# Optimization experiments

Measured on AMD Instinct MI355X. Metric: run time of the kernel, lower is better.

The kernel has to match this reference:

```python
import jax, jax.numpy as jnp
import numpy as np

B, S, D, H = 1, 4096, 1024, 16
HD = D // H

def setup_inputs() -> dict:
    key = jax.random.key(0)
    ks = jax.random.split(key, 6)
    scale = 0.02
    return {
        "x":  jax.random.normal(ks[0], (B, S, D), dtype=jnp.float32),
        "Wq": jax.random.normal(ks[1], (D, D), dtype=jnp.float32) * scale,
        "Wk": jax.random.normal(ks[2], (D, D), dtype=jnp.float32) * scale,
        "Wv": jax.random.normal(ks[3], (D, D), dtype=jnp.float32) * scale,
        "Wo": jax.random.normal(ks[4], (D, D), dtype=jnp.float32) * scale,
        "bo": jnp.zeros((D,), dtype=jnp.float32),
    }

def reference(x, Wq, Wk, Wv, Wo, bo):
    b, s, d = x.shape
    # torch Linear: y = x @ W.T (weights stored [out,in])
    def proj(W):
        return (x @ W.T).reshape(b, s, H, HD).transpose(0, 2, 1, 3)  # [b,h,s,hd]
    q, k, v = proj(Wq), proj(Wk), proj(Wv)
    scores = jnp.einsum('bhqd,bhkd->bhqk', q, k)  # [b,h,s,s]
    causal = jnp.tril(jnp.ones((s, s), dtype=bool))
    scores = jnp.where(causal, scores, -jnp.inf)
    weights = jax.nn.softmax(scores / np.sqrt(HD).astype(np.float32), axis=-1)
    ctx = jnp.einsum('bhqk,bhkd->bhqd', weights, v)
    ctx = ctx.transpose(0, 2, 1, 3).reshape(b, s, d)
    return ctx @ Wo.T + bo
```

## Files before the change

kernel.cpp:

```cpp
#include <hip/hip_runtime.h>
#include <stdint.h>

typedef unsigned short u16;
typedef __attribute__((ext_vector_type(4))) unsigned short u16x4;
typedef __attribute__((ext_vector_type(8))) unsigned short u16x8;
typedef __attribute__((ext_vector_type(8))) __bf16 bf16x8;
typedef __attribute__((ext_vector_type(4))) float f32x4;
typedef __attribute__((ext_vector_type(16))) float f32x16;

#define S_LEN 4096
#define D_DIM 1024
#define NH    16
#define HD    64

__device__ __forceinline__ u16 f2bf(float f) {
  return __builtin_bit_cast(u16, (__bf16)f);
}
__device__ __forceinline__ float bf2f(u16 v) {
  return __builtin_bit_cast(float, (uint32_t)v << 16);
}
__device__ __forceinline__ bf16x8 bc(u16x8 v) { return __builtin_bit_cast(bf16x8, v); }
__device__ __forceinline__ float fexp2(float x) { return __builtin_amdgcn_exp2f(x); }

__device__ __forceinline__ void gload16(const u16* g, u16* l) {
  __builtin_amdgcn_global_load_lds((__attribute__((address_space(1))) void*)g,
                                   (__attribute__((address_space(3))) void*)l, 16, 0, 0);
}

__global__ __launch_bounds__(256) void conv_all_kernel(const float* __restrict__ x,
                                                       const float* __restrict__ Wq,
                                                       const float* __restrict__ Wk,
                                                       const float* __restrict__ Wv,
                                                       const float* __restrict__ Wo,
                                                       u16* __restrict__ Xb, u16* __restrict__ Wqb,
                                                       u16* __restrict__ Wkb, u16* __restrict__ Wvb,
                                                       u16* __restrict__ Wob) {
  int blk = blockIdx.x;
  const float* src;
  u16* dst;
  int i;
  if (blk < 4096) { src = x; dst = Xb; i = blk * 256 + threadIdx.x; }
  else {
    int wi = (blk - 4096) >> 10;
    int lb = (blk - 4096) & 1023;
    src = (wi == 0) ? Wq : (wi == 1) ? Wk : (wi == 2) ? Wv : Wo;
    dst = (wi == 0) ? Wqb : (wi == 1) ? Wkb : (wi == 2) ? Wvb : Wob;
    i = lb * 256 + threadIdx.x;
  }
  f32x4 v = ((const f32x4*)src)[i];
  u16x4 o;
  o[0] = f2bf(v[0]); o[1] = f2bf(v[1]); o[2] = f2bf(v[2]); o[3] = f2bf(v[3]);
  ((u16x4*)dst)[i] = o;
}

__device__ __forceinline__ void gemm_core(const u16* __restrict__ A,
                                          const u16* __restrict__ W,
                                          int m0, int n0, int Kd,
                                          u16* As, u16* Bs, f32x4 acc[4][4]) {
  const int tid  = threadIdx.x;
  const int lane = tid & 63;
  const int wv   = tid >> 6;
  const int wr   = wv >> 1, wc = wv & 1;
  const int b    = lane & 15, quad = lane >> 4;
  const int lrow = lane >> 2;
  const int cg   = ((lane & 3) - (lrow >> 1)) & 3;
  const int goff = ((quad + (b >> 1)) & 3) * 8;

  const u16* ga0 = A + (size_t)(m0 + wv * 16 + lrow) * Kd + cg * 8;
  const u16* ga1 = A + (size_t)(m0 + 64 + wv * 16 + lrow) * Kd + cg * 8;
  const u16* gb0 = W + (size_t)(n0 + wv * 16 + lrow) * Kd + cg * 8;
  const u16* gb1 = W + (size_t)(n0 + 64 + wv * 16 + lrow) * Kd + cg * 8;
  u16* la0 = As + wv * 512;
  u16* la1 = As + 2048 + wv * 512;
  u16* lb0 = Bs + wv * 512;
  u16* lb1 = Bs + 2048 + wv * 512;

  auto stage = [&](int k0, int bsel) {
    gload16(ga0 + k0, la0 + bsel * 4096);
    gload16(ga1 + k0, la1 + bsel * 4096);
    gload16(gb0 + k0, lb0 + bsel * 4096);
    gload16(gb1 + k0, lb1 + bsel * 4096);
  };

  stage(0, 0);
  int buf = 0;
  for (int k0 = 0; k0 < Kd; k0 += 32) {
    __syncthreads();
    if (k0 + 32 < Kd) stage(k0 + 32, buf ^ 1);

    const u16* AB = As + buf * 4096;
    const u16* BB = Bs + buf * 4096;
    u16x8 af[4], bw[4];
#pragma unroll
    for (int i = 0; i < 4; ++i) {
      af[i] = *(const u16x8*)(AB + (wr * 64 + i * 16 + b) * 32 + goff);
      bw[i] = *(const u16x8*)(BB + (wc * 64 + i * 16 + b) * 32 + goff);
    }
#pragma unroll
    for (int i = 0; i < 4; ++i)
#pragma unroll
      for (int j = 0; j < 4; ++j)
        acc[i][j] = __builtin_amdgcn_mfma_f32_16x16x32_bf16(bc(af[i]), bc(bw[j]), acc[i][j], 0, 0, 0);
    buf ^= 1;
  }
}

__global__ __launch_bounds__(256) void gemm_qkv_kernel(const u16* __restrict__ X,
                                                       const u16* __restrict__ Wq,
                                                       const u16* __restrict__ Wk,
                                                       const u16* __restrict__ Wv,
                                                       u16* __restrict__ Q,
                                                       u16* __restrict__ K,
                                                       u16* __restrict__ Vt) {
  __shared__ __align__(16) u16 As[2 * 4096];
  __shared__ __align__(16) u16 Bs[2 * 4096];
  const int z = blockIdx.z;
  const u16* W = (z == 0) ? Wq : (z == 1) ? Wk : Wv;
  const int n0 = blockIdx.x * 128, m0 = blockIdx.y * 128;

  const f32x4 zero4 = {0.f, 0.f, 0.f, 0.f};
  f32x4 acc[4][4];
#pragma unroll
  for (int i = 0; i < 4; ++i)
#pragma unroll
    for (int j = 0; j < 4; ++j) acc[i][j] = zero4;

  gemm_core(X, W, m0, n0, D_DIM, As, Bs, acc);

  const int lane = threadIdx.x & 63;
  const int wv = threadIdx.x >> 6, wr = wv >> 1, wc = wv & 1;
  const int b = lane & 15, quad = lane >> 4;

  if (z < 2) {
    u16* out = (z == 0) ? Q : K;
    const float sc = (z == 0) ? 0.18033688011112042f : 1.0f;
#pragma unroll
    for (int i = 0; i < 4; ++i)
#pragma unroll
      for (int j = 0; j < 4; ++j)
#pragma unroll
        for (int r = 0; r < 4; ++r) {
          int row = m0 + wr * 64 + i * 16 + quad * 4 + r;
          int col = n0 + wc * 64 + j * 16 + b;
          out[(size_t)row * D_DIM + col] = f2bf(acc[i][j][r] * sc);
        }
  } else {
#pragma unroll
    for (int i = 0; i < 4; ++i)
#pragma unroll
      for (int j = 0; j < 4; ++j) {
        int col = n0 + wc * 64 + j * 16 + b;
        int row = m0 + wr * 64 + i * 16 + quad * 4;
        u16x4 vv;
#pragma unroll
        for (int r = 0; r < 4; ++r) vv[r] = f2bf(acc[i][j][r]);
        *(u16x4*)(Vt + (size_t)col * S_LEN + row) = vv;
      }
  }
}

__global__ __launch_bounds__(256) void attn_kernel(const u16* __restrict__ Q,
                                                   const u16* __restrict__ K,
                                                   const u16* __restrict__ Vt,
                                                   u16* __restrict__ Opart,
                                                   float* __restrict__ ml) {
  const int u = (int)gridDim.x - 1 - (int)blockIdx.x;
  const int h = u / 80;
  const int uu = u - h * 80;
  int qt, c;
  if (uu < 8)       { qt = uu;                    c = 0; }
  else if (uu < 24) { qt = 8 + ((uu - 8) >> 1);   c = (uu - 8) & 1; }
  else if (uu < 48) { qt = 16 + (uu - 24) / 3;    c = (uu - 24) % 3; }
  else              { qt = 24 + ((uu - 48) >> 2); c = (uu - 48) & 3; }
  const int t0 = c * 16;
  const int t_end = min(t0 + 16, 2 * qt + 2);
  const int q0 = qt * 128;

  const int tid = threadIdx.x, lane = tid & 63, w = tid >> 6;
  const int half = lane >> 5;
  const int l31 = lane & 31;

  __shared__ __align__(16) u16 Ks[2][4096];
  __shared__ __align__(16) u16 Vts[2][4096];
  __shared__ __align__(16) u16 Ps[4][32 * 72];

  const int sr    = lane >> 3;
  const int srow  = w * 16 + sr;
  const int clog  = ((lane & 7) - sr) & 7;
  const u16* kgb = K + (size_t)srow * D_DIM + h * HD + clog * 8;
  const u16* vgb = Vt + (size_t)(h * HD + srow) * S_LEN + clog * 8;
  u16* const ldk = &Ks[0][0] + w * 16 * 64;
  u16* const ldv = &Vts[0][0] + w * 16 * 64;

  auto stage = [&](int t, int bsel) {
    const u16* kg = kgb + (size_t)t * 64 * D_DIM;
    const u16* vg = vgb + t * 64;
    gload16(kg, ldk + bsel * 4096);
    gload16(kg + 8 * D_DIM, ldk + bsel * 4096 + 512);
    gload16(vg, ldv + bsel * 4096);
    gload16(vg + 8 * S_LEN, ldv + bsel * 4096 + 512);
  };

  u16x8 bq[4];
  {
    const u16* qp = Q + (size_t)(q0 + w * 32 + l31) * D_DIM + h * HD + half * 8;
#pragma unroll
    for (int dt = 0; dt < 4; ++dt) bq[dt] = *(const u16x8*)(qp + dt * 16);
  }

  const f32x16 zero16 = {0.f,0.f,0.f,0.f,0.f,0.f,0.f,0.f,0.f,0.f,0.f,0.f,0.f,0.f,0.f,0.f};
  f32x16 ot[2];
  ot[0] = zero16; ot[1] = zero16;
  float m_run = -3.0e38f, l_run = 0.f;

  u16* const PsW = &Ps[w][0];
  const int qg = q0 + w * 32 + l31;
  const int qg_wmax = q0 + w * 32 + 31;

  stage(t0, 0);
  int buf = 0;

  for (int t = t0; t < t_end; ++t) {
    __syncthreads();
    if (t + 1 < t_end) stage(t + 1, buf ^ 1);

    if (t * 64 <= qg_wmax) {
      const u16* KB = &Ks[buf][0];
      const u16* VB = &Vts[buf][0];

      f32x16 s[2];
      s[0] = zero16; s[1] = zero16;
#pragma unroll
      for (int jt = 0; jt < 2; ++jt) {
        const int row = jt * 32 + l31;
#pragma unroll
        for (int dt = 0; dt < 4; ++dt) {
          u16x8 ak = *(const u16x8*)(KB + row * 64 + (((dt * 2 + half) + row) & 7) * 8);
          s[jt] = __builtin_amdgcn_mfma_f32_32x32x16_bf16(bc(ak), bc(bq[dt]), s[jt], 0, 0, 0);
        }
      }

      if (t * 64 + 63 > qg) {
#pragma unroll
        for (int jt = 0; jt < 2; ++jt) {
          const int kvb = t * 64 + jt * 32 + 4 * half;
#pragma unroll
          for (int e = 0; e < 16; ++e)
            if (kvb + (e & 3) + 8 * (e >> 2) > qg) s[jt][e] = -1.0e30f;
        }
      }

      float mx = -3.0e38f;
#pragma unroll
      for (int jt = 0; jt < 2; ++jt)
#pragma unroll
        for (int e = 0; e < 16; ++e) mx = fmaxf(mx, s[jt][e]);
      mx = fmaxf(mx, __shfl_xor(mx, 32));

      const float mn = fmaxf(m_run, mx);
      const float alpha = fexp2(m_run - mn);
      m_run = mn;

      float sum = 0.f;
#pragma unroll
      for (int jt = 0; jt < 2; ++jt)
#pragma unroll
        for (int g = 0; g < 4; ++g) {
          u16x4 pk;
#pragma unroll
          for (int r = 0; r < 4; ++r) {
            float p = fexp2(s[jt][4 * g + r] - mn);
            sum += p;
            pk[r] = f2bf(p);
          }
          *(u16x4*)(PsW + l31 * 72 + jt * 32 + 4 * half + 8 * g) = pk;
        }
      sum += __shfl_xor(sum, 32);
      l_run = l_run * alpha + sum;

      ot[0] *= alpha;
      ot[1] *= alpha;

#pragma unroll
      for (int kt = 0; kt < 4; ++kt) {
        u16x8 bp = *(const u16x8*)(PsW + l31 * 72 + kt * 16 + half * 8);
#pragma unroll
        for (int dt2 = 0; dt2 < 2; ++dt2) {
          const int row = dt2 * 32 + l31;
          u16x8 av = *(const u16x8*)(VB + row * 64 + (((kt * 2 + half) + row) & 7) * 8);
          ot[dt2] = __builtin_amdgcn_mfma_f32_32x32x16_bf16(bc(av), bc(bp), ot[dt2], 0, 0, 0);
        }
      }
    }
    buf ^= 1;
  }

  const size_t ob = (size_t)u * 8192 + (size_t)(w * 32 + l31) * 64 + 4 * half;
#pragma unroll
  for (int dt2 = 0; dt2 < 2; ++dt2)
#pragma unroll
    for (int g = 0; g < 4; ++g) {
      u16x4 ov;
#pragma unroll
      for (int r = 0; r < 4; ++r) ov[r] = f2bf(ot[dt2][4 * g + r]);
      *(u16x4*)(Opart + ob + dt2 * 32 + 8 * g) = ov;
    }
  if (lane < 32) {
    ml[(size_t)u * 256 + w * 32 + lane]       = m_run;
    ml[(size_t)u * 256 + 128 + w * 32 + lane] = l_run;
  }
}

__global__ __launch_bounds__(256) void attn_combine_kernel(const u16* __restrict__ Opart,
                                                           const float* __restrict__ ml,
                                                           u16* __restrict__ Ctx) {
  const int hq = blockIdx.x;
  const int h = hq >> 6, qt64 = hq & 63;
  const int qt = qt64 >> 1;
  int base;
  if (qt < 8)       base = qt;
  else if (qt < 16) base = 2 * qt - 8;
  else if (qt < 24) base = 3 * qt - 24;
  else              base = 4 * qt - 48;
  base += h * 80;
  const int nc = 1 + (qt >> 3);

  const int tid = threadIdx.x;
  const int row = tid >> 2;
  const int urow = (qt64 & 1) * 64 + row;
  const int dg  = (tid & 3) * 16;

  float M = -3.0e38f;
  for (int ci = 0; ci < nc; ++ci)
    M = fmaxf(M, ml[(size_t)(base + ci) * 256 + urow]);

  float L = 0.f;
  float acc[16];
#pragma unroll
  for (int i = 0; i < 16; ++i) acc[i] = 0.f;

  for (int ci = 0; ci < nc; ++ci) {
    float mp = ml[(size_t)(base + ci) * 256 + urow];
    float lp = ml[(size_t)(base + ci) * 256 + 128 + urow];
    float wgt = fexp2(mp - M);
    L += lp * wgt;
    const u16* op = Opart + (size_t)(base + ci) * 8192 + (size_t)urow * 64 + dg;
    u16x8 v0 = *(const u16x8*)op;
    u16x8 v1 = *(const u16x8*)(op + 8);
#pragma unroll
    for (int i = 0; i < 8; ++i) acc[i] += bf2f(v0[i]) * wgt;
#pragma unroll
    for (int i = 0; i < 8; ++i) acc[i + 8] += bf2f(v1[i]) * wgt;
  }
  const float inv = 1.f / L;
  u16x8 o0, o1;
#pragma unroll
  for (int i = 0; i < 8; ++i) { o0[i] = f2bf(acc[i] * inv); o1[i] = f2bf(acc[i + 8] * inv); }
  u16* dst = Ctx + (size_t)(qt64 * 64 + row) * D_DIM + h * HD + dg;
  *(u16x8*)dst = o0;
  *(u16x8*)(dst + 8) = o1;
}

__global__ __launch_bounds__(256) void gemm_out_kernel(const u16* __restrict__ Ctx,
                                                       const u16* __restrict__ Wo,
                                                       const float* __restrict__ bo,
                                                       float* __restrict__ out) {
  __shared__ __align__(16) u16 As[2 * 4096];
  __shared__ __align__(16) u16 Bs[2 * 4096];
  const int n0 = blockIdx.x * 128, m0 = blockIdx.y * 128;

  const f32x4 zero4 = {0.f, 0.f, 0.f, 0.f};
  f32x4 acc[4][4];
#pragma unroll
  for (int i = 0; i < 4; ++i)
#pragma unroll
    for (int j = 0; j < 4; ++j) acc[i][j] = zero4;

  gemm_core(Ctx, Wo, m0, n0, D_DIM, As, Bs, acc);

  const int lane = threadIdx.x & 63;
  const int wv = threadIdx.x >> 6, wr = wv >> 1, wc = wv & 1;
  const int b = lane & 15, quad = lane >> 4;

#pragma unroll
  for (int j = 0; j < 4; ++j) {
    int col = n0 + wc * 64 + j * 16 + b;
    float bias = bo[col];
#pragma unroll
    for (int i = 0; i < 4; ++i)
#pragma unroll
      for (int r = 0; r < 4; ++r) {
        int row = m0 + wr * 64 + i * 16 + quad * 4 + r;
        out[(size_t)row * D_DIM + col] = acc[i][j][r] + bias;
      }
  }
}

extern "C" void kernel_launch(void* const* d_in, const int* in_sizes, int n_in,
                              void* d_out, int out_size, void* d_ws, size_t ws_size,
                              hipStream_t stream) {
  const float* x  = (const float*)d_in[0];
  const float* Wq = (const float*)d_in[1];
  const float* Wk = (const float*)d_in[2];
  const float* Wv = (const float*)d_in[3];
  const float* Wo = (const float*)d_in[4];
  const float* bo = (const float*)d_in[5];
  float* out = (float*)d_out;

  char* ws = (char*)d_ws;
  const size_t MB = 1u << 20;
  u16*   Xb    = (u16*)(ws + 0 * MB);
  u16*   Wqb   = (u16*)(ws + 8 * MB);
  u16*   Wkb   = (u16*)(ws + 10 * MB);
  u16*   Wvb   = (u16*)(ws + 12 * MB);
  u16*   Wob   = (u16*)(ws + 14 * MB);
  u16*   Qb    = (u16*)(ws + 16 * MB);
  u16*   Kb    = (u16*)(ws + 24 * MB);
  u16*   Vtb   = (u16*)(ws + 32 * MB);
  u16*   Cxb   = (u16*)(ws + 40 * MB);
  u16*   Opart = (u16*)(ws + 48 * MB);
  float* mlbuf = (float*)(ws + 68 * MB);

  conv_all_kernel<<<8192, 256, 0, stream>>>(x, Wq, Wk, Wv, Wo, Xb, Wqb, Wkb, Wvb, Wob);

  gemm_qkv_kernel<<<dim3(D_DIM / 128, S_LEN / 128, 3), 256, 0, stream>>>(
      Xb, Wqb, Wkb, Wvb, Qb, Kb, Vtb);

  attn_kernel<<<dim3(1280), 256, 0, stream>>>(Qb, Kb, Vtb, Opart, mlbuf);

  attn_combine_kernel<<<dim3(1024), 256, 0, stream>>>(Opart, mlbuf, Cxb);

  gemm_out_kernel<<<dim3(D_DIM / 128, S_LEN / 128), 256, 0, stream>>>(Cxb, Wob, bo, out);
}
```

Before: 216.7 us.

## Vectorize GEMM epilogues, stage V transpose via LDS, keep attention P in registers

The Q/K and output GEMMs swap MFMA operand order so each lane holds four consecutive columns, which allows vectorized 8- and 16-byte global stores instead of scalar ones. The V projection now transposes its tile through shared memory so Vt is written with coalesced 16-byte rows. The attention kernel processes one 32-key subtile at a time and exchanges P fragments across half-waves with shuffles instead of a shared-memory round trip, and it adds a launch bound of four blocks per CU. Together these cut store transactions and LDS traffic, at the cost of extra online-softmax rescaling steps and possible register pressure from the occupancy hint.

```diff
diff --git a/kernel.cpp b/kernel.cpp
--- a/kernel.cpp
+++ b/kernel.cpp
@@ -2,8 +2,10 @@
 #include <stdint.h>
 
 typedef unsigned short u16;
+typedef unsigned long long u64;
 typedef __attribute__((ext_vector_type(4))) unsigned short u16x4;
 typedef __attribute__((ext_vector_type(8))) unsigned short u16x8;
+typedef __attribute__((ext_vector_type(2))) unsigned long long u64x2;
 typedef __attribute__((ext_vector_type(8))) __bf16 bf16x8;
 typedef __attribute__((ext_vector_type(4))) float f32x4;
 typedef __attribute__((ext_vector_type(16))) float f32x16;
@@ -53,6 +55,7 @@
   ((u16x4*)dst)[i] = o;
 }
 
+template <bool SWAP>
 __device__ __forceinline__ void gemm_core(const u16* __restrict__ A,
                                           const u16* __restrict__ W,
                                           int m0, int n0, int Kd,
@@ -99,8 +102,12 @@
 #pragma unroll
     for (int i = 0; i < 4; ++i)
 #pragma unroll
-      for (int j = 0; j < 4; ++j)
-        acc[i][j] = __builtin_amdgcn_mfma_f32_16x16x32_bf16(bc(af[i]), bc(bw[j]), acc[i][j], 0, 0, 0);
+      for (int j = 0; j < 4; ++j) {
+        if (SWAP)
+          acc[i][j] = __builtin_amdgcn_mfma_f32_16x16x32_bf16(bc(bw[j]), bc(af[i]), acc[i][j], 0, 0, 0);
+        else
+          acc[i][j] = __builtin_amdgcn_mfma_f32_16x16x32_bf16(bc(af[i]), bc(bw[j]), acc[i][j], 0, 0, 0);
+      }
     buf ^= 1;
   }
 }
@@ -112,8 +119,9 @@
                                                        u16* __restrict__ Q,
                                                        u16* __restrict__ K,
                                                        u16* __restrict__ Vt) {
-  __shared__ __align__(16) u16 As[2 * 4096];
-  __shared__ __align__(16) u16 Bs[2 * 4096];
+  __shared__ __align__(16) u16 SM[16384];
+  u16* As = SM;
+  u16* Bs = SM + 8192;
   const int z = blockIdx.z;
   const u16* W = (z == 0) ? Wq : (z == 1) ? Wk : Wv;
   const int n0 = blockIdx.x * 128, m0 = blockIdx.y * 128;
@@ -125,45 +133,65 @@
 #pragma unroll
     for (int j = 0; j < 4; ++j) acc[i][j] = zero4;
 
-  gemm_core(X, W, m0, n0, D_DIM, As, Bs, acc);
-
-  const int lane = threadIdx.x & 63;
-  const int wv = threadIdx.x >> 6, wr = wv >> 1, wc = wv & 1;
+  const int tid = threadIdx.x;
+  const int lane = tid & 63;
+  const int wv = tid >> 6, wr = wv >> 1, wc = wv & 1;
   const int b = lane & 15, quad = lane >> 4;
 
   if (z < 2) {
+    gemm_core<true>(X, W, m0, n0, D_DIM, As, Bs, acc);
     u16* out = (z == 0) ? Q : K;
     const float sc = (z == 0) ? 0.18033688011112042f : 1.0f;
 #pragma unroll
-    for (int i = 0; i < 4; ++i)
-#pragma unroll
-      for (int j = 0; j < 4; ++j)
-#pragma unroll
-        for (int r = 0; r < 4; ++r) {
-          int row = m0 + wr * 64 + i * 16 + quad * 4 + r;
-          int col = n0 + wc * 64 + j * 16 + b;
-          out[(size_t)row * D_DIM + col] = f2bf(acc[i][j][r] * sc);
+    for (int i = 0; i < 4; ++i) {
+      const int row = m0 + wr * 64 + i * 16 + b;
+#pragma unroll
+      for (int j = 0; j < 4; ++j) {
+        const int col = n0 + wc * 64 + j * 16 + quad * 4;
+        u16x4 ov;
+#pragma unroll
+        for (int r = 0; r < 4; ++r) ov[r] = f2bf(acc[i][j][r] * sc);
+        *(u16x4*)(out + (size_t)row * D_DIM + col) = ov;
+      }
+    }
+  } else {
+    gemm_core<false>(X, W, m0, n0, D_DIM, As, Bs, acc);
+    __syncthreads();
+#pragma unroll
+    for (int p = 0; p < 2; ++p) {
+      if (wc == p) {
+#pragma unroll
+        for (int i = 0; i < 4; ++i) {
+          const int m = wr * 64 + i * 16 + quad * 4;
+          const int g = m >> 3, sub = m & 7;
+#pragma unroll
+          for (int j = 0; j < 4; ++j) {
+            const int c = j * 16 + b;
+            u16x4 ov;
+#pragma unroll
+            for (int r = 0; r < 4; ++r) ov[r] = f2bf(acc[i][j][r]);
+            *(u16x4*)(SM + c * 128 + (((g + c) & 15) * 8) + sub) = ov;
+          }
         }
-  } else {
-#pragma unroll
-    for (int i = 0; i < 4; ++i)
-#pragma unroll
-      for (int j = 0; j < 4; ++j) {
-        int col = n0 + wc * 64 + j * 16 + b;
-        int row = m0 + wr * 64 + i * 16 + quad * 4;
-        u16x4 vv;
-#pragma unroll
-        for (int r = 0; r < 4; ++r) vv[r] = f2bf(acc[i][j][r]);
-        *(u16x4*)(Vt + (size_t)col * S_LEN + row) = vv;
       }
-  }
-}
-
-__global__ __launch_bounds__(256) void attn_kernel(const u16* __restrict__ Q,
-                                                   const u16* __restrict__ K,
-                                                   const u16* __restrict__ Vt,
-                                                   u16* __restrict__ Opart,
-                                                   float* __restrict__ ml) {
+      __syncthreads();
+#pragma unroll
+      for (int cl = 0; cl < 4; ++cl) {
+        const int c2 = cl * 16 + (tid >> 4);
+        const int g2 = tid & 15;
+        u16x8 v = *(const u16x8*)(SM + c2 * 128 + (((g2 + c2) & 15) * 8));
+        *(u16x8*)(Vt + (size_t)(n0 + p * 64 + c2) * S_LEN + m0 + g2 * 8) = v;
+      }
+      __syncthreads();
+    }
+  }
+}
+
+__global__ __launch_bounds__(256, 4) void attn_kernel(const u16* __restrict__ Q,
+                                                      const u16* __restrict__ K,
+                                                      const u16* __restrict__ Vt,
+                                                      u16* __restrict__ Opart,
+                                                      float* __restrict__ ml) {
   const int u = (int)gridDim.x - 1 - (int)blockIdx.x;
   const int h = u / 80;
   const int uu = u - h * 80;
@@ -182,7 +210,6 @@
 
   __shared__ __align__(16) u16 Ks[2][4096];
   __shared__ __align__(16) u16 Vts[2][4096];
-  __shared__ __align__(16) u16 Ps[4][32 * 72];
 
   const int sr    = lane >> 3;
   const int srow  = w * 16 + sr;
@@ -213,7 +240,6 @@
   ot[0] = zero16; ot[1] = zero16;
   float m_run = -3.0e38f, l_run = 0.f;
 
-  u16* const PsW = &Ps[w][0];
   const int qg = q0 + w * 32 + l31;
   const int qg_wmax = q0 + w * 32 + 31;
 
@@ -228,67 +254,62 @@
       const u16* KB = &Ks[buf][0];
       const u16* VB = &Vts[buf][0];
 
-      f32x16 s[2];
-      s[0] = zero16; s[1] = zero16;
 #pragma unroll
       for (int jt = 0; jt < 2; ++jt) {
+        f32x16 s = zero16;
         const int row = jt * 32 + l31;
 #pragma unroll
         for (int dt = 0; dt < 4; ++dt) {
           u16x8 ak = *(const u16x8*)(KB + row * 64 + (((dt * 2 + half) + row) & 7) * 8);
-          s[jt] = __builtin_amdgcn_mfma_f32_32x32x16_bf16(bc(ak), bc(bq[dt]), s[jt], 0, 0, 0);
+          s = __builtin_amdgcn_mfma_f32_32x32x16_bf16(bc(ak), bc(bq[dt]), s, 0, 0, 0);
         }
-      }
-
-      if (t * 64 + 63 > qg) {
-#pragma unroll
-        for (int jt = 0; jt < 2; ++jt) {
-          const int kvb = t * 64 + jt * 32 + 4 * half;
+        const int kvb = t * 64 + jt * 32 + 4 * half;
+        if (kvb + 27 > qg) {
 #pragma unroll
           for (int e = 0; e < 16; ++e)
-            if (kvb + (e & 3) + 8 * (e >> 2) > qg) s[jt][e] = -1.0e30f;
+            if (kvb + (e & 3) + 8 * (e >> 2) > qg) s[e] = -1.0e30f;
         }
-      }
-
-      float mx = -3.0e38f;
-#pragma unroll
-      for (int jt = 0; jt < 2; ++jt)
-#pragma unroll
-        for (int e = 0; e < 16; ++e) mx = fmaxf(mx, s[jt][e]);
-      mx = fmaxf(mx, __shfl_xor(mx, 32));
-
-      const float mn = fmaxf(m_run, mx);
-      const float alpha = fexp2(m_run - mn);
-      m_run = mn;
-
-      float sum = 0.f;
-#pragma unroll
-      for (int jt = 0; jt < 2; ++jt)
+        float mx = -3.0e38f;
+#pragma unroll
+        for (int e = 0; e < 16; ++e) mx = fmaxf(mx, s[e]);
+        mx = fmaxf(mx, __shfl_xor(mx, 32));
+        const float mn = fmaxf(m_run, mx);
+        const float alpha = fexp2(m_run - mn);
+        m_run = mn;
+        float sum = 0.f;
+        u64 pk[4];
 #pragma unroll
         for (int g = 0; g < 4; ++g) {
-          u16x4 pk;
+          u16x4 pkk;
 #pragma unroll
           for (int r = 0; r < 4; ++r) {
-            float p = fexp2(s[jt][4 * g + r] - mn);
+            float p = fexp2(s[4 * g + r] - mn);
             sum += p;
-            pk[r] = f2bf(p);
+            pkk[r] = f2bf(p);
           }
-          *(u16x4*)(PsW + l31 * 72 + jt * 32 + 4 * half + 8 * g) = pk;
+          pk[g] = __builtin_bit_cast(u64, pkk);
         }
-      sum += __shfl_xor(sum, 32);
-      l_run = l_run * alpha + sum;
-
-      ot[0] *= alpha;
-      ot[1] *= alpha;
-
-#pragma unroll
-      for (int kt = 0; kt < 4; ++kt) {
-        u16x8 bp = *(const u16x8*)(PsW + l31 * 72 + kt * 16 + half * 8);
-#pragma unroll
-        for (int dt2 = 0; dt2 < 2; ++dt2) {
-          const int row = dt2 * 32 + l31;
-          u16x8 av = *(const u16x8*)(VB + row * 64 + (((kt * 2 + half) + row) & 7) * 8);
-          ot[dt2] = __builtin_amdgcn_mfma_f32_32x32x16_bf16(bc(av), bc(bp), ot[dt2], 0, 0, 0);
+        sum += __shfl_xor(sum, 32);
+        l_run = l_run * alpha + sum;
+        ot[0] *= alpha;
+        ot[1] *= alpha;
+
+#pragma unroll
+        for (int kt2 = 0; kt2 < 2; ++kt2) {
+          const int ge = kt2 * 2;
+          u64 send = half ? pk[ge] : pk[ge + 1];
+          u64 recv = __shfl_xor(send, 32);
+          u64 lo = half ? recv : pk[ge];
+          u64 hi = half ? pk[ge + 1] : recv;
+          u64x2 bp2 = {lo, hi};
+          u16x8 bp = __builtin_bit_cast(u16x8, bp2);
+          const int kt = jt * 2 + kt2;
+#pragma unroll
+          for (int dt2 = 0; dt2 < 2; ++dt2) {
+            const int row2 = dt2 * 32 + l31;
+            u16x8 av = *(const u16x8*)(VB + row2 * 64 + (((kt * 2 + half) + row2) & 7) * 8);
+            ot[dt2] = __builtin_amdgcn_mfma_f32_32x32x16_bf16(bc(av), bc(bp), ot[dt2], 0, 0, 0);
+          }
         }
       }
     }
@@ -376,7 +397,7 @@
 #pragma unroll
     for (int j = 0; j < 4; ++j) acc[i][j] = zero4;
 
-  gemm_core(Ctx, Wo, m0, n0, D_DIM, As, Bs, acc);
+  gemm_core<true>(Ctx, Wo, m0, n0, D_DIM, As, Bs, acc);
 
   const int lane = threadIdx.x & 63;
   const int wv = threadIdx.x >> 6, wr = wv >> 1, wc = wv & 1;
@@ -384,15 +405,14 @@
 
 #pragma unroll
   for (int j = 0; j < 4; ++j) {
-    int col = n0 + wc * 64 + j * 16 + b;
-    float bias = bo[col];
-#pragma unroll
-    for (int i = 0; i < 4; ++i)
-#pragma unroll
-      for (int r = 0; r < 4; ++r) {
-        int row = m0 + wr * 64 + i * 16 + quad * 4 + r;
-        out[(size_t)row * D_DIM + col] = acc[i][j][r] + bias;
-      }
+    const int col = n0 + wc * 64 + j * 16 + quad * 4;
+    const f32x4 bias = *(const f32x4*)(bo + col);
+#pragma unroll
+    for (int i = 0; i < 4; ++i) {
+      const int row = m0 + wr * 64 + i * 16 + b;
+      f32x4 ov = acc[i][j] + bias;
+      *(f32x4*)(out + (size_t)row * D_DIM + col) = ov;
+    }
   }
 }
 
```

Result: slower. 223.0 us (+2.9%).
